# Performance work log

Hardware: AMD Instinct MI355X
Metric: run time of the kernel (lower is better)

## Reference

```python
import jax, jax.numpy as jnp
import numpy as np

BETA = 0.25
K = 1024   # codebook_size
D = 64     # emb_dim


def setup_inputs() -> dict:
    key = jax.random.key(0)
    k1, k2 = jax.random.split(key)
    z_e = jax.random.normal(k1, (32, 64, 64, D), dtype=jnp.float32)
    codebook = jax.random.normal(k2, (K, D), dtype=jnp.float32) * 0.05
    return {"z_e": z_e, "codebook": codebook}


def reference(z_e, codebook):
    sg = jax.lax.stop_gradient
    k, d = codebook.shape
    z = z_e.reshape(-1, d)                                   # [N, D]
    # squared euclidean distances: ||z||^2 + ||e||^2 - 2 z.e
    z_sq = jnp.sum(z * z, axis=1, keepdims=True)             # [N, 1]
    e_sq = jnp.sum(codebook * codebook, axis=1)              # [K]
    distances = z_sq + e_sq[None, :] - 2.0 * (z @ codebook.T)  # [N, K]
    indices = jnp.argmin(distances, axis=1)                  # [N] int
    z_q = jnp.take(codebook, indices, axis=0).reshape(z_e.shape)
    commitment = jnp.mean((sg(z_e) - z_q) ** 2)
    codebook_loss = jnp.mean((z_e - sg(z_q)) ** 2)
    z_q_st = z_e + sg(z_q - z_e)
    loss_vq = codebook_loss + BETA * commitment
    # perplexity (no-grad in original)
    n = z.shape[0]
    counts = jnp.zeros((k,), dtype=jnp.float32).at[indices].add(1.0)
    avg_probs = sg(counts / n)
    perplexity = jnp.exp(-jnp.sum(avg_probs * jnp.log(avg_probs + 1e-12)))
    return z_q_st, indices.reshape(z_e.shape[:-1]), loss_vq, perplexity
```

## Files before the change

kernel.cpp:

```cpp
#include <hip/hip_runtime.h>

#define N_VEC   131072
#define D       64
#define KCODES  1024
#define NT      64
#define BLK     256
#define VPB     128
#define CH      4
#define NCH     (NT / CH)

typedef __attribute__((ext_vector_type(8))) short bf16x8;
typedef __attribute__((ext_vector_type(4))) float f32x4;

#define GLD16(dst, src) __builtin_amdgcn_global_load_lds(                      \
    (const __attribute__((address_space(1))) void*)(src),                      \
    (__attribute__((address_space(3))) void*)(dst), 16, 0, 0)


__device__ __forceinline__ float4 f4fma(float4 a, float4 b, float4 c) {
    return make_float4(fmaf(a.x, b.x, c.x), fmaf(a.y, b.y, c.y),
                       fmaf(a.z, b.z, c.z), fmaf(a.w, b.w, c.w));
}
__device__ __forceinline__ float f4rsum(float4 a) {
    return (a.x + a.y) + (a.z + a.w);
}
__device__ __forceinline__ unsigned short f2bf(float f) {
    union { float f; unsigned u; } x; x.f = f;
    unsigned r = x.u + 0x7FFFu + ((x.u >> 16) & 1u);
    return (unsigned short)(r >> 16);
}
__device__ __forceinline__ float bf2f(unsigned short h) {
    union { unsigned u; float f; } x; x.u = ((unsigned)h) << 16;
    return x.f;
}
__device__ __forceinline__ int   f_as_i(float f) { union { float f; int i; } x; x.f = f; return x.i; }
__device__ __forceinline__ float i_as_f(int i)   { union { int i; float f; } x; x.i = i; return x.f; }

__global__ void prep_kernel(const float* __restrict__ cb, float* __restrict__ esq,
                            bf16x8* __restrict__ afrag, float4* __restrict__ efrag) {
    __shared__ float sesq[64];
    const int tid = threadIdx.x;
    const int c0  = blockIdx.x * 64;
    if (tid < 64) {
        const float4* c4 = reinterpret_cast<const float4*>(cb + (size_t)(c0 + tid) * D);
        float4 p = make_float4(0.f, 0.f, 0.f, 0.f);
        #pragma unroll
        for (int i = 0; i < 16; ++i) { float4 v = c4[i]; p = f4fma(v, v, p); }
        float e = f4rsum(p);
        esq[c0 + tid] = e;
        sesq[tid] = e;
    }
    __syncthreads();
    const int tt = tid >> 6;
    const int L  = tid & 63;
    const int t  = blockIdx.x * 4 + tt;
    const int g  = L >> 4;
    const int r  = t * 16 + (L & 15);
    #pragma unroll
    for (int ks = 0; ks < 2; ++ks) {
        const float* src = cb + (size_t)r * D + ks * 32 + g * 8;
        bf16x8 h, l;
        #pragma unroll
        for (int e = 0; e < 8; ++e) {
            float f = src[e];
            unsigned short hb = f2bf(f);
            float lo = f - bf2f(hb);
            h[e] = (short)hb;
            l[e] = (short)f2bf(lo);
        }
        afrag[(t * 4 + ks * 2 + 0) * 64 + L] = h;
        afrag[(t * 4 + ks * 2 + 1) * 64 + L] = l;
    }
    float4 ef;
    ef.x = -0.5f * sesq[tt * 16 + g * 4 + 0];
    ef.y = -0.5f * sesq[tt * 16 + g * 4 + 1];
    ef.z = -0.5f * sesq[tt * 16 + g * 4 + 2];
    ef.w = -0.5f * sesq[tt * 16 + g * 4 + 3];
    efrag[t * 64 + L] = ef;
}

__device__ __forceinline__ void insd(float ov, int og,
                                     float& v0, float& v1, float& v2,
                                     int& g0, int& g1, int& g2) {
    bool b1 = (ov > v0) || (ov == v0 && og < g0);
    bool b2 = (ov > v1) || (ov == v1 && og < g1);
    bool b3 = (ov > v2) || (ov == v2 && og < g2);
    float nv2 = b2 ? v1 : (b3 ? ov : v2);
    int   ng2 = b2 ? g1 : (b3 ? og : g2);
    float nv1 = b1 ? v0 : (b2 ? ov : v1);
    int   ng1 = b1 ? g0 : (b2 ? og : g1);
    v0 = b1 ? ov : v0;
    g0 = b1 ? og : g0;
    v1 = nv1; g1 = ng1; v2 = nv2; g2 = ng2;
}

__launch_bounds__(BLK)
__global__ void vq_fused(const float* __restrict__ z_e, const float* __restrict__ cb,
                         const float* __restrict__ esq,
                         const float4* __restrict__ afrag4, const float4* __restrict__ efrag,
                         float* __restrict__ zq_out, float* __restrict__ idx_out,
                         float* __restrict__ sse, int* __restrict__ counts) {
    __shared__ float4 scb[2][CH * 4 * 64];
    __shared__ float4 sef[2][CH * 64];
    char* ovl = (char*)&scb[0][0];
    int  (*scand)[3] = reinterpret_cast<int(*)[3]>(ovl);
    float* sZsq = reinterpret_cast<float*>(ovl + 2048);
    float* sS1  = reinterpret_cast<float*>(ovl + 2560);
    float* sS2  = reinterpret_cast<float*>(ovl + 3072);
    float* sC2  = reinterpret_cast<float*>(ovl + 3584);
    float* sred = reinterpret_cast<float*>(ovl + 4096);

    const int tid  = threadIdx.x;
    const int wave = tid >> 6;
    const int L    = tid & 63;
    const int lrow = L & 15;
    const int g    = L >> 4;
    const size_t vbase = (size_t)blockIdx.x * VPB + wave * 32;

    bf16x8 zhi[2][2], zlo[2][2];
    #pragma unroll
    for (int b = 0; b < 2; ++b) {
        #pragma unroll
        for (int ks = 0; ks < 2; ++ks) {
            const float* zp = z_e + (vbase + b * 16 + lrow) * D + ks * 32 + g * 8;
            float4 u0 = *reinterpret_cast<const float4*>(zp);
            float4 u1 = *reinterpret_cast<const float4*>(zp + 4);
            float fv[8] = {u0.x, u0.y, u0.z, u0.w, u1.x, u1.y, u1.z, u1.w};
            bf16x8 h, l;
            #pragma unroll
            for (int e = 0; e < 8; ++e) {
                unsigned short hb = f2bf(fv[e]);
                float lo = fv[e] - bf2f(hb);
                h[e] = (short)hb;
                l[e] = (short)f2bf(lo);
            }
            zhi[b][ks] = h; zlo[b][ks] = l;
        }
    }

    float m1[2], m2[2], m3[2];
    #pragma unroll
    for (int b = 0; b < 2; ++b) { m1[b] = m2[b] = m3[b] = -INFINITY; }

    #pragma unroll
    for (int i = 0; i < 4; ++i) GLD16(&scb[0][i * BLK + tid], afrag4 + i * BLK + tid);
    GLD16(&sef[0][tid], efrag + tid);

    int cur = 0;
    for (int c = 0; c < NCH; ++c) {
        __syncthreads();
        if (c + 1 < NCH) {
            const float4* gA = afrag4 + (size_t)(c + 1) * (CH * 4 * 64);
            const float4* gE = efrag + (size_t)(c + 1) * (CH * 64);
            #pragma unroll
            for (int i = 0; i < 4; ++i) GLD16(&scb[cur ^ 1][i * BLK + tid], gA + i * BLK + tid);
            GLD16(&sef[cur ^ 1][tid], gE + tid);
        }

        #pragma unroll
        for (int tt = 0; tt < CH; ++tt) {
            const int t = c * CH + tt;
            const bf16x8* fr = reinterpret_cast<const bf16x8*>(&scb[cur][tt * 256]);
            bf16x8 Ah0 = fr[0 * 64 + L];
            bf16x8 Al0 = fr[1 * 64 + L];
            bf16x8 Ah1 = fr[2 * 64 + L];
            bf16x8 Al1 = fr[3 * 64 + L];
            f32x4 einit;
            {
                float4 ef = sef[cur][tt * 64 + L];
                einit[0] = ef.x; einit[1] = ef.y; einit[2] = ef.z; einit[3] = ef.w;
            }

            #pragma unroll
            for (int b = 0; b < 2; ++b) {
                f32x4 acc;
                acc = __builtin_amdgcn_mfma_f32_16x16x32_bf16(Ah0, zhi[b][0], einit, 0, 0, 0);
                acc = __builtin_amdgcn_mfma_f32_16x16x32_bf16(Ah0, zlo[b][0], acc, 0, 0, 0);
                acc = __builtin_amdgcn_mfma_f32_16x16x32_bf16(Al0, zhi[b][0], acc, 0, 0, 0);
                acc = __builtin_amdgcn_mfma_f32_16x16x32_bf16(Ah1, zhi[b][1], acc, 0, 0, 0);
                acc = __builtin_amdgcn_mfma_f32_16x16x32_bf16(Ah1, zlo[b][1], acc, 0, 0, 0);
                acc = __builtin_amdgcn_mfma_f32_16x16x32_bf16(Al1, zhi[b][1], acc, 0, 0, 0);

                #pragma unroll
                for (int j = 0; j < 4; ++j) {
                    int komp = 255 - ((t << 2) | j);
                    float pd = i_as_f((f_as_i(acc[j]) & 0xFFFFFF00) | komp);
                    float mn = fminf(m2[b], pd);
                    float md = __builtin_amdgcn_fmed3f(m1[b], pd, m2[b]);
                    m1[b] = fmaxf(m1[b], pd);
                    m2[b] = md;
                    m3[b] = fmaxf(m3[b], mn);
                }
            }
        }
        cur ^= 1;
    }

    __syncthreads();

    #pragma unroll
    for (int b = 0; b < 2; ++b) {
        float v0, v1, v2; int g0, g1, g2;
        {
            int p0 = f_as_i(m1[b]), p1 = f_as_i(m2[b]), p2 = f_as_i(m3[b]);
            int c0 = 255 - (p0 & 255), c1 = 255 - (p1 & 255), c2 = 255 - (p2 & 255);
            v0 = i_as_f(p0 & ~255); g0 = (c0 >> 2) * 16 + g * 4 + (c0 & 3);
            v1 = i_as_f(p1 & ~255); g1 = (c1 >> 2) * 16 + g * 4 + (c1 & 3);
            v2 = i_as_f(p2 & ~255); g2 = (c2 >> 2) * 16 + g * 4 + (c2 & 3);
        }
        #pragma unroll
        for (int m = 16; m <= 32; m <<= 1) {
            float ov0 = __shfl_xor(v0, m), ov1 = __shfl_xor(v1, m), ov2 = __shfl_xor(v2, m);
            int   og0 = __shfl_xor(g0, m), og1 = __shfl_xor(g1, m), og2 = __shfl_xor(g2, m);
            insd(ov0, og0, v0, v1, v2, g0, g1, g2);
            insd(ov1, og1, v0, v1, v2, g0, g1, g2);
            insd(ov2, og2, v0, v1, v2, g0, g1, g2);
        }
        if (g == 0) {
            int lv = wave * 32 + b * 16 + lrow;
            scand[lv][0] = g0; scand[lv][1] = g1; scand[lv][2] = g2;
        }
    }
    __syncthreads();

    const int vid = tid & (VPB - 1);
    const int sub = tid >> 7;
    const size_t n = (size_t)blockIdx.x * VPB + vid;
    {
        const float4* z4 = reinterpret_cast<const float4*>(z_e + n * D);
        if (sub == 0) {
            int ci0 = scand[vid][0];
            const float4* cp0 = reinterpret_cast<const float4*>(cb + (size_t)ci0 * D);
            float4 pq = make_float4(0.f, 0.f, 0.f, 0.f);
            float4 s0 = pq;
            #pragma unroll
            for (int i = 0; i < 16; ++i) {
                float4 zz = z4[i];
                pq = f4fma(zz, zz, pq);
                s0 = f4fma(zz, cp0[i], s0);
            }
            sZsq[vid] = f4rsum(pq);
            sS1[vid]  = f4rsum(s0);
        } else {
            int ci1 = scand[vid][1];
            int ci2 = scand[vid][2];
            const float4* cp1 = reinterpret_cast<const float4*>(cb + (size_t)ci1 * D);
            const float4* cp2 = reinterpret_cast<const float4*>(cb + (size_t)ci2 * D);
            float4 s1 = make_float4(0.f, 0.f, 0.f, 0.f);
            float4 s2 = s1;
            #pragma unroll
            for (int i = 0; i < 16; ++i) {
                float4 zz = z4[i];
                s1 = f4fma(zz, cp1[i], s1);
                s2 = f4fma(zz, cp2[i], s2);
            }
            sS2[vid] = f4rsum(s1);
            sC2[vid] = f4rsum(s2);
        }
    }
    __syncthreads();

    float v = 0.f;
    if (sub == 0) {
        int ci0 = scand[vid][0], ci1 = scand[vid][1], ci2 = scand[vid][2];
        float zsq = sZsq[vid];
        float d0 = fmaf(-2.0f, sS1[vid], zsq + esq[ci0]);
        float d1 = fmaf(-2.0f, sS2[vid], zsq + esq[ci1]);
        float d2 = fmaf(-2.0f, sC2[vid], zsq + esq[ci2]);
        float bd = d0; int bi = ci0;
        if (d1 < bd || (d1 == bd && ci1 < bi)) { bd = d1; bi = ci1; }
        if (d2 < bd || (d2 == bd && ci2 < bi)) { bd = d2; bi = ci2; }
        idx_out[n] = (float)bi;
        atomicAdd(&counts[bi], 1);
        scand[vid][0] = bi;
        v = bd;
    }
    #pragma unroll
    for (int off = 32; off > 0; off >>= 1) v += __shfl_down(v, off);
    if ((tid & 63) == 0) sred[tid >> 6] = v;
    __syncthreads();
    if (tid == 0) atomicAdd(sse, (sred[0] + sred[1]) + (sred[2] + sred[3]));

    const float4* cb4 = reinterpret_cast<const float4*>(cb);
    float4* zq4 = reinterpret_cast<float4*>(zq_out) + (size_t)blockIdx.x * (VPB * 16);
    #pragma unroll
    for (int i = 0; i < 8; ++i) {
        int mi  = i * BLK + tid;
        int vec = mi >> 4;
        int e   = mi & 15;
        zq4[mi] = cb4[(size_t)scand[vec][0] * 16 + e];
    }
}

__global__ void finalize_kernel(const int* __restrict__ counts, const float* __restrict__ sse,
                                float* __restrict__ out_loss, float* __restrict__ out_perp) {
    __shared__ float red[256];
    int tid = threadIdx.x;
    float hsum = 0.f;
    for (int k = tid; k < KCODES; k += 256) {
        float p = (float)counts[k] / (float)N_VEC;
        hsum += p * logf(p + 1e-12f);
    }
    red[tid] = hsum;
    __syncthreads();
    for (int s = 128; s > 0; s >>= 1) {
        if (tid < s) red[tid] += red[tid + s];
        __syncthreads();
    }
    if (tid == 0) {
        out_loss[0] = 1.25f * sse[0] / 8388608.0f;
        out_perp[0] = expf(-red[0]);
    }
}

extern "C" void kernel_launch(void* const* d_in, const int* in_sizes, int n_in,
                              void* d_out, int out_size, void* d_ws, size_t ws_size,
                              hipStream_t stream) {
    const float* z_e = (const float*)d_in[0];
    const float* cb  = (const float*)d_in[1];

    float* out  = (float*)d_out;
    float* zq   = out;
    float* idxo = out + (size_t)N_VEC * D;
    float* loss = idxo + N_VEC;
    float* perp = loss + 1;

    char* ws = (char*)d_ws;
    int*    counts = (int*)ws;
    float*  sse    = (float*)(ws + 4096);
    float*  esq    = (float*)(ws + 5120);
    float4* efrag  = (float4*)(ws + 16384);
    bf16x8* afrag  = (bf16x8*)(ws + 81920);

    hipMemsetAsync(d_ws, 0, 5120, stream);
    prep_kernel<<<16, 256, 0, stream>>>(cb, esq, afrag, efrag);
    vq_fused<<<N_VEC / VPB, BLK, 0, stream>>>(z_e, cb, esq, (const float4*)afrag, efrag,
                                              zq, idxo, sse, counts);
    finalize_kernel<<<1, 256, 0, stream>>>(counts, sse, loss, perp);
}
```

Baseline: 103.7 us.

## Triple-buffer codebook staging with prefetch distance two and explicit vmcnt waits

Moves the codebook-fragment staging from double to triple buffering in LDS. Chunks are now prefetched two steps ahead, and the full __syncthreads is replaced by an s_waitcnt vmcnt(5) plus s_barrier, so the loads for the next chunk can stay in flight while the current one is consumed. This hides more global load latency at the cost of about 50% more LDS for the staging buffers, which may reduce occupancy. It also depends on the hand-written vmcnt count matching exactly five outstanding loads per stage.

```diff
diff --git a/kernel.cpp b/kernel.cpp
--- a/kernel.cpp
+++ b/kernel.cpp
@@ -100,8 +100,8 @@
                          const float4* __restrict__ afrag4, const float4* __restrict__ efrag,
                          float* __restrict__ zq_out, float* __restrict__ idx_out,
                          float* __restrict__ sse, int* __restrict__ counts) {
-    __shared__ float4 scb[2][CH * 4 * 64];
-    __shared__ float4 sef[2][CH * 64];
+    __shared__ float4 scb[3][CH * 4 * 64];
+    __shared__ float4 sef[3][CH * 64];
     char* ovl = (char*)&scb[0][0];
     int  (*scand)[3] = reinterpret_cast<int(*)[3]>(ovl);
     float* sZsq = reinterpret_cast<float*>(ovl + 2048);
@@ -142,32 +142,43 @@
     #pragma unroll
     for (int b = 0; b < 2; ++b) { m1[b] = m2[b] = m3[b] = -INFINITY; }
 
-    #pragma unroll
-    for (int i = 0; i < 4; ++i) GLD16(&scb[0][i * BLK + tid], afrag4 + i * BLK + tid);
-    GLD16(&sef[0][tid], efrag + tid);
-
-    int cur = 0;
+    #define STAGE(cc, bi) do {                                                  \
+        const float4* gA_ = afrag4 + (size_t)(cc) * (CH * 4 * 64);              \
+        const float4* gE_ = efrag + (size_t)(cc) * (CH * 64);                   \
+        GLD16(&scb[bi][0 * BLK + tid], gA_ + 0 * BLK + tid);                    \
+        GLD16(&scb[bi][1 * BLK + tid], gA_ + 1 * BLK + tid);                    \
+        GLD16(&scb[bi][2 * BLK + tid], gA_ + 2 * BLK + tid);                    \
+        GLD16(&scb[bi][3 * BLK + tid], gA_ + 3 * BLK + tid);                    \
+        GLD16(&sef[bi][tid], gE_ + tid);                                        \
+    } while (0)
+
+    STAGE(0, 0);
+    STAGE(1, 1);
+
     for (int c = 0; c < NCH; ++c) {
-        __syncthreads();
-        if (c + 1 < NCH) {
-            const float4* gA = afrag4 + (size_t)(c + 1) * (CH * 4 * 64);
-            const float4* gE = efrag + (size_t)(c + 1) * (CH * 64);
-            #pragma unroll
-            for (int i = 0; i < 4; ++i) GLD16(&scb[cur ^ 1][i * BLK + tid], gA + i * BLK + tid);
-            GLD16(&sef[cur ^ 1][tid], gE + tid);
-        }
-
+        if (c < NCH - 1) { asm volatile("s_waitcnt vmcnt(5)" ::: "memory"); }
+        else             { asm volatile("s_waitcnt vmcnt(0)" ::: "memory"); }
+        __builtin_amdgcn_sched_barrier(0);
+        __builtin_amdgcn_s_barrier();
+        __builtin_amdgcn_sched_barrier(0);
+
+        if (c + 2 < NCH) {
+            const int bn = (c + 2) % 3;
+            STAGE(c + 2, bn);
+        }
+
+        const int bi = c % 3;
         #pragma unroll
         for (int tt = 0; tt < CH; ++tt) {
             const int t = c * CH + tt;
-            const bf16x8* fr = reinterpret_cast<const bf16x8*>(&scb[cur][tt * 256]);
+            const bf16x8* fr = reinterpret_cast<const bf16x8*>(&scb[bi][tt * 256]);
             bf16x8 Ah0 = fr[0 * 64 + L];
             bf16x8 Al0 = fr[1 * 64 + L];
             bf16x8 Ah1 = fr[2 * 64 + L];
             bf16x8 Al1 = fr[3 * 64 + L];
             f32x4 einit;
             {
-                float4 ef = sef[cur][tt * 64 + L];
+                float4 ef = sef[bi][tt * 64 + L];
                 einit[0] = ef.x; einit[1] = ef.y; einit[2] = ef.z; einit[3] = ef.w;
             }
 
@@ -193,7 +204,6 @@
                 }
             }
         }
-        cur ^= 1;
     }
 
     __syncthreads();
```

After: 115.8 us. +11.7%, slower.
